# Optimization experiments

Measured on AMD Instinct MI355X. Metric: run time of the kernel, lower is better.

The kernel has to match this reference:

```python
import jax, jax.numpy as jnp
import numpy as np

B, N, M, D, H = 4, 2048, 2048, 1024, 16
HD = D // H


def setup_inputs() -> dict:
    key = jax.random.key(0)
    ks = jax.random.split(key, 16)
    s = 1.0 / np.sqrt(D)
    inp = {
        "Q": jax.random.normal(ks[0], (B, N, D), jnp.float32),
        "K": jax.random.normal(ks[1], (B, M, D), jnp.float32),
        "V": jax.random.normal(ks[2], (B, M, D), jnp.float32),
        "attn_bias": jax.random.normal(ks[3], (B, N, M), jnp.float32),
        "mask": jax.random.randint(ks[4], (B, M), 0, 2).astype(bool),
        # linear params (torch nn.Linear: y = x @ W.T + b)
        "Wq": jax.random.uniform(ks[5], (D, D), jnp.float32, -s, s),
        "bq": jax.random.uniform(ks[6], (D,), jnp.float32, -s, s),
        "Wk": jax.random.uniform(ks[7], (D, D), jnp.float32, -s, s),
        "bk": jax.random.uniform(ks[8], (D,), jnp.float32, -s, s),
        "Wv": jax.random.uniform(ks[9], (D, D), jnp.float32, -s, s),
        "bv": jax.random.uniform(ks[10], (D,), jnp.float32, -s, s),
        "Wo": jax.random.uniform(ks[11], (D, D), jnp.float32, -s, s),
        "bo": jax.random.uniform(ks[12], (D,), jnp.float32, -s, s),
    }
    return inp


def reference(Q, K, V, attn_bias, mask, Wq, bq, Wk, bk, Wv, bv, Wo, bo):
    b, n, d = Q.shape
    m = K.shape[1]
    # bias (B,N,M) -> (B,1,N,M); mask (B,M) True = masked out (-inf)
    bias = attn_bias[:, None, :, :]
    bias = jnp.where(mask[:, None, None, :], -jnp.inf, bias)
    # projections, split heads: (B, H, len, head_dim)
    q = (Q @ Wq.T + bq).reshape(b, n, H, HD).transpose(0, 2, 1, 3)
    k = (K @ Wk.T + bk).reshape(b, m, H, HD).transpose(0, 2, 1, 3)
    v = (V @ Wv.T + bv).reshape(b, m, H, HD).transpose(0, 2, 1, 3)
    scale = 1.0 / np.sqrt(HD).astype(np.float32)
    attn = jnp.einsum("bhid,bhjd->bhij", q * scale, k) + bias
    attn = jax.nn.softmax(attn, axis=-1)
    out = jnp.einsum("bhij,bhjd->bhid", attn, v)
    out = out.transpose(0, 2, 1, 3).reshape(b, n, d)
    return out @ Wo.T + bo
```

## Files before the change

kernel.cpp:

```cpp
#include <hip/hip_runtime.h>
#include <hip/hip_bf16.h>

#define Bq 4
#define Nq 2048
#define Mq 2048
#define Dq 1024
#define Hq 16

typedef __attribute__((ext_vector_type(8))) short short8;
typedef __attribute__((ext_vector_type(4))) short short4v;
typedef __attribute__((ext_vector_type(4))) float floatx4;
typedef __attribute__((ext_vector_type(16))) float floatx16;
typedef __attribute__((ext_vector_type(4))) unsigned uint4v;

static __device__ __forceinline__ short f2bf(float f) {
    __hip_bfloat16 h = __float2bfloat16(f);
    short r;
    __builtin_memcpy(&r, &h, 2);
    return r;
}
static __device__ __forceinline__ float bf2f(short s) {
    unsigned u = ((unsigned)(unsigned short)s) << 16;
    float f;
    __builtin_memcpy(&f, &u, 4);
    return f;
}
static __device__ __forceinline__ unsigned cvtpk_bf16(float lo, float hi) {
    unsigned r;
    asm("v_cvt_pk_bf16_f32 %0, %1, %2" : "=v"(r) : "v"(lo), "v"(hi));
    return r;
}
static __device__ __forceinline__ void swap32(unsigned &a, unsigned &b) {
    asm("v_permlane32_swap_b32 %0, %1" : "+v"(a), "+v"(b));
}
static __device__ __forceinline__ void gld16(const void* g, void* l) {
    __builtin_amdgcn_global_load_lds(
        (const __attribute__((address_space(1))) unsigned int*)g,
        (__attribute__((address_space(3))) unsigned int*)l, 16, 0, 0);
}

__global__ void bias_prep(const float* __restrict__ bias, const int* __restrict__ mask,
                          short* __restrict__ out)
{
    const long i = ((long)blockIdx.x * 256 + threadIdx.x) * 4;
    const int m = (int)(i & (Mq - 1));
    const int b = (int)(i >> 22);
    floatx4 v = *(const floatx4*)(bias + i);
    short4v o;
#pragma unroll
    for (int e = 0; e < 4; ++e) {
        const float t = v[e] + (mask[b * Mq + m + e] ? -1e38f : 0.0f);
        o[e] = f2bf(t);
    }
    *(short4v*)(out + i) = o;
}

template<bool A_BF16, int OMODE>
__global__ __launch_bounds__(256, 2)
void gemm_bt(const void* __restrict__ Ap, const float* __restrict__ Bp,
             const float* __restrict__ biasp, void* __restrict__ Cp, int K, float scale)
{
    __shared__ short As[128 * 32];
    __shared__ short Bs[128 * 32];
    short8* As8 = (short8*)As;
    short8* Bs8 = (short8*)Bs;

    const int tid = threadIdx.x;
    const int lane = tid & 63;
    const int wid = tid >> 6;
    const int wr = wid >> 1, wc = wid & 1;
    const int g = lane >> 4, c = lane & 15;
    const long row0 = (long)blockIdx.x * 128;
    const int col0 = blockIdx.y * 128;

    const int srow = tid >> 1;
    const int sk = (tid & 1) * 16;

    floatx4 acc[4][4];
#pragma unroll
    for (int i = 0; i < 4; ++i)
#pragma unroll
        for (int j = 0; j < 4; ++j) acc[i][j] = (floatx4)0.0f;

    for (int kt = 0; kt < K; kt += 32) {
        short8 a0, a1, b0, b1;
        if constexpr (A_BF16) {
            const short* ap = (const short*)Ap + (row0 + srow) * (long)K + kt + sk;
            a0 = *(const short8*)ap;
            a1 = *(const short8*)(ap + 8);
        } else {
            const float* ap = (const float*)Ap + (row0 + srow) * (long)K + kt + sk;
            floatx4 f0 = *(const floatx4*)ap,       f1 = *(const floatx4*)(ap + 4),
                    f2 = *(const floatx4*)(ap + 8), f3 = *(const floatx4*)(ap + 12);
#pragma unroll
            for (int e = 0; e < 4; ++e) {
                a0[e] = f2bf(f0[e]); a0[e + 4] = f2bf(f1[e]);
                a1[e] = f2bf(f2[e]); a1[e + 4] = f2bf(f3[e]);
            }
        }
        {
            const float* bp = Bp + (col0 + srow) * (long)K + kt + sk;
            floatx4 f0 = *(const floatx4*)bp,       f1 = *(const floatx4*)(bp + 4),
                    f2 = *(const floatx4*)(bp + 8), f3 = *(const floatx4*)(bp + 12);
#pragma unroll
            for (int e = 0; e < 4; ++e) {
                b0[e] = f2bf(f0[e]); b0[e + 4] = f2bf(f1[e]);
                b1[e] = f2bf(f2[e]); b1[e + 4] = f2bf(f3[e]);
            }
        }
        const int u0 = sk >> 3;
        const int sw = (srow >> 1) & 3;
        As8[srow * 4 + ((u0)     ^ sw)] = a0;
        As8[srow * 4 + ((u0 + 1) ^ sw)] = a1;
        Bs8[srow * 4 + ((u0)     ^ sw)] = b0;
        Bs8[srow * 4 + ((u0 + 1) ^ sw)] = b1;
        __syncthreads();

        short8 af[4], bfq[4];
#pragma unroll
        for (int fm = 0; fm < 4; ++fm) {
            const int r = wr * 64 + fm * 16 + c;
            af[fm] = As8[r * 4 + (g ^ ((r >> 1) & 3))];
        }
#pragma unroll
        for (int fn = 0; fn < 4; ++fn) {
            const int cc = wc * 64 + fn * 16 + c;
            bfq[fn] = Bs8[cc * 4 + (g ^ ((cc >> 1) & 3))];
        }
#pragma unroll
        for (int fm = 0; fm < 4; ++fm)
#pragma unroll
            for (int fn = 0; fn < 4; ++fn)
                acc[fm][fn] = __builtin_amdgcn_mfma_f32_16x16x32_bf16(af[fm], bfq[fn], acc[fm][fn], 0, 0, 0);
        __syncthreads();
    }

#pragma unroll
    for (int fn = 0; fn < 4; ++fn) {
        const int ccol = col0 + wc * 64 + fn * 16 + c;
        const float bv = biasp[ccol];
#pragma unroll
        for (int fm = 0; fm < 4; ++fm) {
            const long r0 = row0 + wr * 64 + fm * 16 + g * 4;
#pragma unroll
            for (int reg = 0; reg < 4; ++reg) {
                const float val = (acc[fm][fn][reg] + bv) * scale;
                const long rr = r0 + reg;
                if constexpr (OMODE == 0) {
                    ((float*)Cp)[rr * 1024 + ccol] = val;
                } else if constexpr (OMODE == 1) {
                    ((short*)Cp)[rr * 1024 + ccol] = f2bf(val);
                } else {
                    const long idx = ((long)(rr >> 11) * Dq + ccol) * (long)Mq + (rr & (Mq - 1));
                    ((short*)Cp)[idx] = f2bf(val);
                }
            }
        }
    }
}

__global__ __launch_bounds__(512, 2)
void attn_fused(const short* __restrict__ qg_, const short* __restrict__ kg_,
                const short* __restrict__ vtg, const short* __restrict__ bmg,
                short* __restrict__ outg)
{
    __shared__ __align__(16) short k_lds[64 * 64];
    __shared__ __align__(16) short v_lds[64 * 64];

    const int tid = threadIdx.x;
    const int lane = tid & 63;
    const int w = tid >> 6;
    const int hi = lane >> 5;
    const int q31 = lane & 31;

    const int blk = blockIdx.x;
    const int xcd = blk & 7, s = blk >> 3;
    const int grp = xcd * 2 + (s >> 4);
    const int b = grp >> 2, qt = grp & 3;
    const int h = s & 15;

    const long qbase = (long)b * Nq + qt * 512 + w * 64;

    short8 qf[2][4];
#pragma unroll
    for (int qg = 0; qg < 2; ++qg)
#pragma unroll
        for (int ks = 0; ks < 4; ++ks)
            qf[qg][ks] = *(const short8*)(qg_ + (qbase + qg * 32 + q31) * Dq + h * 64 + ks * 16 + hi * 8);

    floatx16 oa[2][2];
    float m_s[2], l_s[2];
#pragma unroll
    for (int qg = 0; qg < 2; ++qg) {
        m_s[qg] = -1e37f; l_s[qg] = 0.0f;
        oa[qg][0] = (floatx16)0.0f; oa[qg][1] = (floatx16)0.0f;
    }

    const int sr = tid >> 3;
    const int su = (tid & 7) ^ (sr & 7);
    const char* ksrc0 = (const char*)(kg_ + ((long)b * Mq + sr) * Dq + h * 64 + su * 8);
    const char* vsrc0 = (const char*)(vtg + ((long)b * Dq + h * 64 + sr) * Mq + su * 8);
    void* kdst = (void*)((char*)k_lds + w * 1024);
    void* vdst = (void*)((char*)v_lds + w * 1024);

    for (int kt = 0; kt < 32; ++kt) {
        const long j0 = (long)kt * 64;
        gld16(ksrc0 + j0 * (Dq * 2), kdst);
        gld16(vsrc0 + j0 * 2, vdst);
        __syncthreads();

        short8 kf[2][4];
#pragma unroll
        for (int kg = 0; kg < 2; ++kg)
#pragma unroll
            for (int ks = 0; ks < 4; ++ks) {
                const int r = kg * 32 + q31;
                const int up = (2 * ks + hi) ^ (r & 7);
                kf[kg][ks] = *(const short8*)((const char*)k_lds + r * 128 + up * 16);
            }
        floatx16 sa[2][2];
#pragma unroll
        for (int qg = 0; qg < 2; ++qg)
#pragma unroll
            for (int kg = 0; kg < 2; ++kg) {
                sa[qg][kg] = (floatx16)0.0f;
#pragma unroll
                for (int ks = 0; ks < 4; ++ks)
                    sa[qg][kg] = __builtin_amdgcn_mfma_f32_32x32x16_bf16(kf[kg][ks], qf[qg][ks], sa[qg][kg], 0, 0, 0);
            }

        short8 vf[2][4];
#pragma unroll
        for (int dg = 0; dg < 2; ++dg)
#pragma unroll
            for (int ks = 0; ks < 4; ++ks) {
                const int r = dg * 32 + q31;
                const int up = (2 * ks + hi) ^ (r & 7);
                vf[dg][ks] = *(const short8*)((const char*)v_lds + r * 128 + up * 16);
            }

#pragma unroll
        for (int qg = 0; qg < 2; ++qg) {
            const short* brow = bmg + (qbase + qg * 32 + q31) * Mq + j0;
            float p[32];
#pragma unroll
            for (int kg = 0; kg < 2; ++kg)
#pragma unroll
                for (int Qh = 0; Qh < 4; ++Qh) {
                    short4v bb = *(const short4v*)(brow + kg * 32 + Qh * 8 + hi * 4);
#pragma unroll
                    for (int e = 0; e < 4; ++e)
                        p[kg * 16 + Qh * 4 + e] = sa[qg][kg][Qh * 4 + e] + bf2f(bb[e]);
                }
            float pm = p[0];
#pragma unroll
            for (int i = 1; i < 32; ++i) pm = fmaxf(pm, p[i]);
            pm = fmaxf(pm, __shfl_xor(pm, 32));
            if (!__all(pm <= m_s[qg] + 8.0f)) {
                const float mn = fmaxf(m_s[qg], pm);
                const float al = __expf(m_s[qg] - mn);
                l_s[qg] *= al;
                oa[qg][0] *= al; oa[qg][1] *= al;
                m_s[qg] = mn;
            }
            float rs = 0.0f;
#pragma unroll
            for (int i = 0; i < 32; ++i) { p[i] = __expf(p[i] - m_s[qg]); rs += p[i]; }
            rs += __shfl_xor(rs, 32);
            l_s[qg] += rs;

            uint4v pw[4];
#pragma unroll
            for (int kg = 0; kg < 2; ++kg) {
                unsigned w0 = cvtpk_bf16(p[kg * 16 + 0], p[kg * 16 + 1]);
                unsigned w1 = cvtpk_bf16(p[kg * 16 + 2], p[kg * 16 + 3]);
                unsigned w2 = cvtpk_bf16(p[kg * 16 + 4], p[kg * 16 + 5]);
                unsigned w3 = cvtpk_bf16(p[kg * 16 + 6], p[kg * 16 + 7]);
                swap32(w0, w2); swap32(w1, w3);
                pw[kg * 2][0] = w0; pw[kg * 2][1] = w1; pw[kg * 2][2] = w2; pw[kg * 2][3] = w3;
                unsigned w4 = cvtpk_bf16(p[kg * 16 + 8],  p[kg * 16 + 9]);
                unsigned w5 = cvtpk_bf16(p[kg * 16 + 10], p[kg * 16 + 11]);
                unsigned w6 = cvtpk_bf16(p[kg * 16 + 12], p[kg * 16 + 13]);
                unsigned w7 = cvtpk_bf16(p[kg * 16 + 14], p[kg * 16 + 15]);
                swap32(w4, w6); swap32(w5, w7);
                pw[kg * 2 + 1][0] = w4; pw[kg * 2 + 1][1] = w5; pw[kg * 2 + 1][2] = w6; pw[kg * 2 + 1][3] = w7;
            }
#pragma unroll
            for (int dg = 0; dg < 2; ++dg)
#pragma unroll
                for (int ks = 0; ks < 4; ++ks)
                    oa[qg][dg] = __builtin_amdgcn_mfma_f32_32x32x16_bf16(
                        vf[dg][ks], __builtin_bit_cast(short8, pw[ks]), oa[qg][dg], 0, 0, 0);
        }
        __syncthreads();
    }

#pragma unroll
    for (int qg = 0; qg < 2; ++qg) {
        const float invl = 1.0f / l_s[qg];
        short* op = outg + (qbase + qg * 32 + q31) * Dq + h * 64;
#pragma unroll
        for (int dg = 0; dg < 2; ++dg)
#pragma unroll
            for (int Qh = 0; Qh < 4; ++Qh) {
                short4v t;
#pragma unroll
                for (int e = 0; e < 4; ++e)
                    t[e] = f2bf(oa[qg][dg][Qh * 4 + e] * invl);
                *(short4v*)(op + dg * 32 + Qh * 8 + hi * 4) = t;
            }
    }
}

extern "C" void kernel_launch(void* const* d_in, const int* in_sizes, int n_in,
                              void* d_out, int out_size, void* d_ws, size_t ws_size,
                              hipStream_t stream)
{
    const float* Q    = (const float*)d_in[0];
    const float* K    = (const float*)d_in[1];
    const float* V    = (const float*)d_in[2];
    const float* bias = (const float*)d_in[3];
    const int*   mask = (const int*)d_in[4];
    const float* Wq   = (const float*)d_in[5];
    const float* bq   = (const float*)d_in[6];
    const float* Wk   = (const float*)d_in[7];
    const float* bk   = (const float*)d_in[8];
    const float* Wv   = (const float*)d_in[9];
    const float* bv   = (const float*)d_in[10];
    const float* Wo   = (const float*)d_in[11];
    const float* bo   = (const float*)d_in[12];

    const size_t SZ = (size_t)Bq * Nq * Dq;
    short* q_ws  = (short*)d_ws;
    short* k_ws  = q_ws  + (size_t)Bq * Nq * Dq;
    short* vt_ws = k_ws  + (size_t)Bq * Mq * Dq;
    short* a_ws  = vt_ws + (size_t)Bq * Mq * Dq;
    short* bm_ws = a_ws  + (size_t)Bq * Nq * Dq;
    (void)SZ; (void)ws_size;

    bias_prep<<<dim3((Bq * Nq * Mq) / 4 / 256), dim3(256), 0, stream>>>(bias, mask, bm_ws);

    dim3 grid(64, 8);
    gemm_bt<false, 1><<<grid, 256, 0, stream>>>(Q, Wq, bq, q_ws, Dq, 0.125f);
    gemm_bt<false, 1><<<grid, 256, 0, stream>>>(K, Wk, bk, k_ws, Dq, 1.0f);
    gemm_bt<false, 2><<<grid, 256, 0, stream>>>(V, Wv, bv, vt_ws, Dq, 1.0f);
    attn_fused<<<dim3(256), dim3(512), 0, stream>>>(q_ws, k_ws, vt_ws, bm_ws, a_ws);
    gemm_bt<true, 0><<<grid, 256, 0, stream>>>(a_ws, Wo, bo, d_out, Dq, 1.0f);
}
```

Before: 359.4 us.

## Double-buffer GEMM and attention, pre-convert weights, batch QKV, use exp2 softmax

The four weight matrices are converted to bf16 once in a separate kernel, and the three QKV projections are batched into a single launch over a z grid dimension. The GEMM now double-buffers shared memory, staging weights with global-to-LDS loads so the next tile is fetched during the current MFMAs. The attention kernel is reorganised into 256-thread blocks that each process 32 queries per wave, with double-buffered K/V tiles, the bias loads hoisted ahead of the MFMAs, and tree reductions for max and sum. Softmax switches to exp2 by folding log2(e) into the Q scale and the bias, and the rescale threshold is relaxed. The trade-off is an extra conversion launch, higher LDS use, and different occupancy.

Measured after the change: 342.4 us. 1.05x faster.

```diff
diff --git a/kernel.cpp b/kernel.cpp
--- a/kernel.cpp
+++ b/kernel.cpp
@@ -33,6 +33,11 @@
 static __device__ __forceinline__ void swap32(unsigned &a, unsigned &b) {
     asm("v_permlane32_swap_b32 %0, %1" : "+v"(a), "+v"(b));
 }
+static __device__ __forceinline__ float exp2_fast(float x) {
+    float r;
+    asm("v_exp_f32 %0, %1" : "=v"(r) : "v"(x));
+    return r;
+}
 static __device__ __forceinline__ void gld16(const void* g, void* l) {
     __builtin_amdgcn_global_load_lds(
         (const __attribute__((address_space(1))) unsigned int*)g,
@@ -42,28 +47,56 @@
 __global__ void bias_prep(const float* __restrict__ bias, const int* __restrict__ mask,
                           short* __restrict__ out)
 {
-    const long i = ((long)blockIdx.x * 256 + threadIdx.x) * 4;
+    const long i = ((long)blockIdx.x * 256 + threadIdx.x) * 8;
     const int m = (int)(i & (Mq - 1));
     const int b = (int)(i >> 22);
-    floatx4 v = *(const floatx4*)(bias + i);
-    short4v o;
+    floatx4 f0 = *(const floatx4*)(bias + i);
+    floatx4 f1 = *(const floatx4*)(bias + i + 4);
+    const int* mp = mask + b * Mq + m;
+    short8 o;
 #pragma unroll
     for (int e = 0; e < 4; ++e) {
-        const float t = v[e] + (mask[b * Mq + m + e] ? -1e38f : 0.0f);
-        o[e] = f2bf(t);
-    }
-    *(short4v*)(out + i) = o;
-}
-
-template<bool A_BF16, int OMODE>
-__global__ __launch_bounds__(256, 2)
-void gemm_bt(const void* __restrict__ Ap, const float* __restrict__ Bp,
-             const float* __restrict__ biasp, void* __restrict__ Cp, int K, float scale)
+        o[e]     = mp[e]     ? f2bf(-1e38f) : f2bf(f0[e] * 1.44269504f);
+        o[e + 4] = mp[e + 4] ? f2bf(-1e38f) : f2bf(f1[e] * 1.44269504f);
+    }
+    *(short8*)(out + i) = o;
+}
+
+__global__ void cvt_w(const float* __restrict__ w0, const float* __restrict__ w1,
+                      const float* __restrict__ w2, const float* __restrict__ w3,
+                      short* __restrict__ out)
 {
-    __shared__ short As[128 * 32];
-    __shared__ short Bs[128 * 32];
-    short8* As8 = (short8*)As;
-    short8* Bs8 = (short8*)Bs;
+    const int z = blockIdx.y;
+    const float* s = (z == 0) ? w0 : (z == 1) ? w1 : (z == 2) ? w2 : w3;
+    short* d = out + (size_t)z * (Dq * Dq);
+    const int i = (blockIdx.x * 256 + threadIdx.x) * 8;
+    floatx4 f0 = *(const floatx4*)(s + i);
+    floatx4 f1 = *(const floatx4*)(s + i + 4);
+    short8 o;
+#pragma unroll
+    for (int e = 0; e < 4; ++e) { o[e] = f2bf(f0[e]); o[e + 4] = f2bf(f1[e]); }
+    *(short8*)(d + i) = o;
+}
+
+struct GB {
+    const void* A[3];
+    const short* W[3];
+    const float* bias[3];
+    void* C[3];
+    float scale[3];
+    int omode[3];
+};
+
+template<bool ABF>
+__global__ __launch_bounds__(256, 3)
+void gemm_bt(GB gb, int K)
+{
+    __shared__ __align__(16) short As[2][128 * 32];
+    __shared__ __align__(16) short Bs[2][128 * 32];
+
+    const int z = blockIdx.z;
+    const char* Ap = (const char*)gb.A[z];
+    const short* Wp = gb.W[z];
 
     const int tid = threadIdx.x;
     const int lane = tid & 63;
@@ -75,6 +108,9 @@
 
     const int srow = tid >> 1;
     const int sk = (tid & 1) * 16;
+    const int R0 = tid >> 2;
+    const int ub = (tid & 3) ^ ((R0 >> 1) & 3);
+    const short* bsrc = Wp + ((long)col0 + R0) * K + ub * 8;
 
     floatx4 acc[4][4];
 #pragma unroll
@@ -82,14 +118,18 @@
 #pragma unroll
         for (int j = 0; j < 4; ++j) acc[i][j] = (floatx4)0.0f;
 
-    for (int kt = 0; kt < K; kt += 32) {
-        short8 a0, a1, b0, b1;
-        if constexpr (A_BF16) {
-            const short* ap = (const short*)Ap + (row0 + srow) * (long)K + kt + sk;
-            a0 = *(const short8*)ap;
-            a1 = *(const short8*)(ap + 8);
+    {
+        char* d0 = (char*)Bs + wid * 1024;
+        gld16(bsrc, d0);
+        gld16(bsrc + 64L * K, d0 + 4096);
+    }
+    {
+        short8 a0, a1;
+        if constexpr (ABF) {
+            const short* ap = (const short*)Ap + (row0 + srow) * (long)K + sk;
+            a0 = *(const short8*)ap; a1 = *(const short8*)(ap + 8);
         } else {
-            const float* ap = (const float*)Ap + (row0 + srow) * (long)K + kt + sk;
+            const float* ap = (const float*)Ap + (row0 + srow) * (long)K + sk;
             floatx4 f0 = *(const floatx4*)ap,       f1 = *(const floatx4*)(ap + 4),
                     f2 = *(const floatx4*)(ap + 8), f3 = *(const floatx4*)(ap + 12);
 #pragma unroll
@@ -98,24 +138,33 @@
                 a1[e] = f2bf(f2[e]); a1[e + 4] = f2bf(f3[e]);
             }
         }
-        {
-            const float* bp = Bp + (col0 + srow) * (long)K + kt + sk;
-            floatx4 f0 = *(const floatx4*)bp,       f1 = *(const floatx4*)(bp + 4),
-                    f2 = *(const floatx4*)(bp + 8), f3 = *(const floatx4*)(bp + 12);
-#pragma unroll
-            for (int e = 0; e < 4; ++e) {
-                b0[e] = f2bf(f0[e]); b0[e + 4] = f2bf(f1[e]);
-                b1[e] = f2bf(f2[e]); b1[e + 4] = f2bf(f3[e]);
-            }
-        }
-        const int u0 = sk >> 3;
-        const int sw = (srow >> 1) & 3;
+        short8* As8 = (short8*)As;
+        const int u0 = sk >> 3, sw = (srow >> 1) & 3;
         As8[srow * 4 + ((u0)     ^ sw)] = a0;
         As8[srow * 4 + ((u0 + 1) ^ sw)] = a1;
-        Bs8[srow * 4 + ((u0)     ^ sw)] = b0;
-        Bs8[srow * 4 + ((u0 + 1) ^ sw)] = b1;
-        __syncthreads();
-
+    }
+    __syncthreads();
+
+    int buf = 0;
+    for (int kt = 0; kt < K; kt += 32) {
+        const bool nlast = (kt + 32 < K);
+        floatx4 f0, f1, f2, f3;
+        short8 s0, s1;
+        if (nlast) {
+            char* d0 = (char*)Bs + (buf ^ 1) * 8192 + wid * 1024;
+            gld16(bsrc + kt + 32, d0);
+            gld16(bsrc + 64L * K + kt + 32, d0 + 4096);
+            if constexpr (ABF) {
+                const short* ap = (const short*)Ap + (row0 + srow) * (long)K + kt + 32 + sk;
+                s0 = *(const short8*)ap; s1 = *(const short8*)(ap + 8);
+            } else {
+                const float* ap = (const float*)Ap + (row0 + srow) * (long)K + kt + 32 + sk;
+                f0 = *(const floatx4*)ap;       f1 = *(const floatx4*)(ap + 4);
+                f2 = *(const floatx4*)(ap + 8); f3 = *(const floatx4*)(ap + 12);
+            }
+        }
+        short8* As8 = (short8*)((char*)As + buf * 8192);
+        short8* Bs8 = (short8*)((char*)Bs + buf * 8192);
         short8 af[4], bfq[4];
 #pragma unroll
         for (int fm = 0; fm < 4; ++fm) {
@@ -132,40 +181,60 @@
 #pragma unroll
             for (int fn = 0; fn < 4; ++fn)
                 acc[fm][fn] = __builtin_amdgcn_mfma_f32_16x16x32_bf16(af[fm], bfq[fn], acc[fm][fn], 0, 0, 0);
+        if (nlast) {
+            short8 a0, a1;
+            if constexpr (ABF) { a0 = s0; a1 = s1; }
+            else {
+#pragma unroll
+                for (int e = 0; e < 4; ++e) {
+                    a0[e] = f2bf(f0[e]); a0[e + 4] = f2bf(f1[e]);
+                    a1[e] = f2bf(f2[e]); a1[e + 4] = f2bf(f3[e]);
+                }
+            }
+            short8* An8 = (short8*)((char*)As + (buf ^ 1) * 8192);
+            const int u0 = sk >> 3, sw = (srow >> 1) & 3;
+            An8[srow * 4 + ((u0)     ^ sw)] = a0;
+            An8[srow * 4 + ((u0 + 1) ^ sw)] = a1;
+        }
         __syncthreads();
-    }
-
+        buf ^= 1;
+    }
+
+    const float sc = gb.scale[z];
+    const float* bp = gb.bias[z];
+    const int om = gb.omode[z];
+    void* Cp = gb.C[z];
 #pragma unroll
     for (int fn = 0; fn < 4; ++fn) {
         const int ccol = col0 + wc * 64 + fn * 16 + c;
-        const float bv = biasp[ccol];
+        const float bv = bp[ccol];
 #pragma unroll
         for (int fm = 0; fm < 4; ++fm) {
             const long r0 = row0 + wr * 64 + fm * 16 + g * 4;
 #pragma unroll
             for (int reg = 0; reg < 4; ++reg) {
-                const float val = (acc[fm][fn][reg] + bv) * scale;
+                const float val = (acc[fm][fn][reg] + bv) * sc;
                 const long rr = r0 + reg;
-                if constexpr (OMODE == 0) {
-                    ((float*)Cp)[rr * 1024 + ccol] = val;
-                } else if constexpr (OMODE == 1) {
-                    ((short*)Cp)[rr * 1024 + ccol] = f2bf(val);
-                } else {
+                if (om == 0) {
+                    ((short*)Cp)[rr * Dq + ccol] = f2bf(val);
+                } else if (om == 1) {
                     const long idx = ((long)(rr >> 11) * Dq + ccol) * (long)Mq + (rr & (Mq - 1));
                     ((short*)Cp)[idx] = f2bf(val);
+                } else {
+                    ((float*)Cp)[rr * Dq + ccol] = val;
                 }
             }
         }
     }
 }
 
-__global__ __launch_bounds__(512, 2)
+__global__ __launch_bounds__(256, 4)
 void attn_fused(const short* __restrict__ qg_, const short* __restrict__ kg_,
                 const short* __restrict__ vtg, const short* __restrict__ bmg,
                 short* __restrict__ outg)
 {
-    __shared__ __align__(16) short k_lds[64 * 64];
-    __shared__ __align__(16) short v_lds[64 * 64];
+    __shared__ __align__(16) short k_lds[2][64 * 64];
+    __shared__ __align__(16) short v_lds[2][64 * 64];
 
     const int tid = threadIdx.x;
     const int lane = tid & 63;
@@ -174,142 +243,154 @@
     const int q31 = lane & 31;
 
     const int blk = blockIdx.x;
-    const int xcd = blk & 7, s = blk >> 3;
-    const int grp = xcd * 2 + (s >> 4);
-    const int b = grp >> 2, qt = grp & 3;
-    const int h = s & 15;
-
-    const long qbase = (long)b * Nq + qt * 512 + w * 64;
-
-    short8 qf[2][4];
-#pragma unroll
-    for (int qg = 0; qg < 2; ++qg)
-#pragma unroll
-        for (int ks = 0; ks < 4; ++ks)
-            qf[qg][ks] = *(const short8*)(qg_ + (qbase + qg * 32 + q31) * Dq + h * 64 + ks * 16 + hi * 8);
-
-    floatx16 oa[2][2];
-    float m_s[2], l_s[2];
-#pragma unroll
-    for (int qg = 0; qg < 2; ++qg) {
-        m_s[qg] = -1e37f; l_s[qg] = 0.0f;
-        oa[qg][0] = (floatx16)0.0f; oa[qg][1] = (floatx16)0.0f;
-    }
+    const int bh = blk & 63;
+    const int qt = blk >> 6;
+    const int b = bh >> 4, h = bh & 15;
+
+    const long qbase = (long)b * Nq + qt * 128 + w * 32;
+
+    short8 qf[4];
+#pragma unroll
+    for (int ks = 0; ks < 4; ++ks)
+        qf[ks] = *(const short8*)(qg_ + (qbase + q31) * Dq + h * 64 + ks * 16 + hi * 8);
+
+    floatx16 oa[2];
+    oa[0] = (floatx16)0.0f; oa[1] = (floatx16)0.0f;
+    float m_s = -1e37f, l_s = 0.0f;
 
     const int sr = tid >> 3;
     const int su = (tid & 7) ^ (sr & 7);
-    const char* ksrc0 = (const char*)(kg_ + ((long)b * Mq + sr) * Dq + h * 64 + su * 8);
-    const char* vsrc0 = (const char*)(vtg + ((long)b * Dq + h * 64 + sr) * Mq + su * 8);
-    void* kdst = (void*)((char*)k_lds + w * 1024);
-    void* vdst = (void*)((char*)v_lds + w * 1024);
-
+    const char* ksrc = (const char*)(kg_ + ((long)b * Mq + sr) * Dq + h * 64 + su * 8);
+    const char* vsrc = (const char*)(vtg + ((long)b * Dq + h * 64 + sr) * Mq + su * 8);
+
+#define STAGE(bf, kt2) do {                                                   \
+        const long j0b = (long)(kt2) * 64;                                    \
+        char* kd = (char*)k_lds + (bf) * 8192 + w * 1024;                     \
+        char* vd = (char*)v_lds + (bf) * 8192 + w * 1024;                     \
+        gld16(ksrc + j0b * (Dq * 2), kd);                                     \
+        gld16(ksrc + (j0b + 32) * (Dq * 2), kd + 4096);                       \
+        gld16(vsrc + j0b * 2, vd);                                            \
+        gld16(vsrc + 32L * Mq * 2 + j0b * 2, vd + 4096);                      \
+    } while (0)
+
+    STAGE(0, 0);
+    __syncthreads();
+
+    int buf = 0;
     for (int kt = 0; kt < 32; ++kt) {
-        const long j0 = (long)kt * 64;
-        gld16(ksrc0 + j0 * (Dq * 2), kdst);
-        gld16(vsrc0 + j0 * 2, vdst);
-        __syncthreads();
-
-        short8 kf[2][4];
+        if (kt < 31) STAGE(buf ^ 1, kt + 1);
+        const short* brow = bmg + (qbase + q31) * Mq + (long)kt * 64;
+        short4v bb[8];
 #pragma unroll
         for (int kg = 0; kg < 2; ++kg)
+#pragma unroll
+            for (int Qh = 0; Qh < 4; ++Qh)
+                bb[kg * 4 + Qh] = *(const short4v*)(brow + kg * 32 + Qh * 8 + hi * 4);
+
+        const char* kb = (const char*)k_lds + buf * 8192;
+        const char* vb = (const char*)v_lds + buf * 8192;
+
+        floatx16 sa[2];
+#pragma unroll
+        for (int kg = 0; kg < 2; ++kg) {
+            short8 kf[4];
 #pragma unroll
             for (int ks = 0; ks < 4; ++ks) {
                 const int r = kg * 32 + q31;
                 const int up = (2 * ks + hi) ^ (r & 7);
-                kf[kg][ks] = *(const short8*)((const char*)k_lds + r * 128 + up * 16);
-            }
-        floatx16 sa[2][2];
-#pragma unroll
-        for (int qg = 0; qg < 2; ++qg)
-#pragma unroll
-            for (int kg = 0; kg < 2; ++kg) {
-                sa[qg][kg] = (floatx16)0.0f;
-#pragma unroll
-                for (int ks = 0; ks < 4; ++ks)
-                    sa[qg][kg] = __builtin_amdgcn_mfma_f32_32x32x16_bf16(kf[kg][ks], qf[qg][ks], sa[qg][kg], 0, 0, 0);
-            }
-
-        short8 vf[2][4];
-#pragma unroll
-        for (int dg = 0; dg < 2; ++dg)
+                kf[ks] = *(const short8*)(kb + r * 128 + up * 16);
+            }
+            sa[kg] = (floatx16)0.0f;
+#pragma unroll
+            for (int ks = 0; ks < 4; ++ks)
+                sa[kg] = __builtin_amdgcn_mfma_f32_32x32x16_bf16(kf[ks], qf[ks], sa[kg], 0, 0, 0);
+        }
+
+        float p[32];
+#pragma unroll
+        for (int kg = 0; kg < 2; ++kg)
+#pragma unroll
+            for (int Qh = 0; Qh < 4; ++Qh) {
+                const short4v bv4 = bb[kg * 4 + Qh];
+#pragma unroll
+                for (int e = 0; e < 4; ++e)
+                    p[kg * 16 + Qh * 4 + e] = sa[kg][Qh * 4 + e] + bf2f(bv4[e]);
+            }
+        float t16[16];
+#pragma unroll
+        for (int i = 0; i < 16; ++i) t16[i] = fmaxf(p[2 * i], p[2 * i + 1]);
+#pragma unroll
+        for (int i = 0; i < 8; ++i) t16[i] = fmaxf(t16[2 * i], t16[2 * i + 1]);
+        t16[0] = fmaxf(fmaxf(fmaxf(t16[0], t16[1]), fmaxf(t16[2], t16[3])),
+                       fmaxf(fmaxf(t16[4], t16[5]), fmaxf(t16[6], t16[7])));
+        const float pm = fmaxf(t16[0], __shfl_xor(t16[0], 32));
+        if (!__all(pm <= m_s + 11.5f)) {
+            const float mn = fmaxf(m_s, pm);
+            const float al = exp2_fast(m_s - mn);
+            l_s *= al;
+            oa[0] *= al; oa[1] *= al;
+            m_s = mn;
+        }
+#pragma unroll
+        for (int i = 0; i < 32; ++i) p[i] = exp2_fast(p[i] - m_s);
+        float s16[16];
+#pragma unroll
+        for (int i = 0; i < 16; ++i) s16[i] = p[2 * i] + p[2 * i + 1];
+#pragma unroll
+        for (int i = 0; i < 8; ++i) s16[i] = s16[2 * i] + s16[2 * i + 1];
+        float rs = ((s16[0] + s16[1]) + (s16[2] + s16[3])) +
+                   ((s16[4] + s16[5]) + (s16[6] + s16[7]));
+        rs += __shfl_xor(rs, 32);
+        l_s += rs;
+
+        uint4v pw[4];
+#pragma unroll
+        for (int kg = 0; kg < 2; ++kg) {
+            unsigned w0 = cvtpk_bf16(p[kg * 16 + 0], p[kg * 16 + 1]);
+            unsigned w1 = cvtpk_bf16(p[kg * 16 + 2], p[kg * 16 + 3]);
+            unsigned w2 = cvtpk_bf16(p[kg * 16 + 4], p[kg * 16 + 5]);
+            unsigned w3 = cvtpk_bf16(p[kg * 16 + 6], p[kg * 16 + 7]);
+            swap32(w0, w2); swap32(w1, w3);
+            pw[kg * 2][0] = w0; pw[kg * 2][1] = w1; pw[kg * 2][2] = w2; pw[kg * 2][3] = w3;
+            unsigned w4 = cvtpk_bf16(p[kg * 16 + 8],  p[kg * 16 + 9]);
+            unsigned w5 = cvtpk_bf16(p[kg * 16 + 10], p[kg * 16 + 11]);
+            unsigned w6 = cvtpk_bf16(p[kg * 16 + 12], p[kg * 16 + 13]);
+            unsigned w7 = cvtpk_bf16(p[kg * 16 + 14], p[kg * 16 + 15]);
+            swap32(w4, w6); swap32(w5, w7);
+            pw[kg * 2 + 1][0] = w4; pw[kg * 2 + 1][1] = w5; pw[kg * 2 + 1][2] = w6; pw[kg * 2 + 1][3] = w7;
+        }
+
+#pragma unroll
+        for (int dg = 0; dg < 2; ++dg) {
+            short8 vf[4];
 #pragma unroll
             for (int ks = 0; ks < 4; ++ks) {
                 const int r = dg * 32 + q31;
                 const int up = (2 * ks + hi) ^ (r & 7);
-                vf[dg][ks] = *(const short8*)((const char*)v_lds + r * 128 + up * 16);
-            }
-
-#pragma unroll
-        for (int qg = 0; qg < 2; ++qg) {
-            const short* brow = bmg + (qbase + qg * 32 + q31) * Mq + j0;
-            float p[32];
-#pragma unroll
-            for (int kg = 0; kg < 2; ++kg)
-#pragma unroll
-                for (int Qh = 0; Qh < 4; ++Qh) {
-                    short4v bb = *(const short4v*)(brow + kg * 32 + Qh * 8 + hi * 4);
-#pragma unroll
-                    for (int e = 0; e < 4; ++e)
-                        p[kg * 16 + Qh * 4 + e] = sa[qg][kg][Qh * 4 + e] + bf2f(bb[e]);
-                }
-            float pm = p[0];
-#pragma unroll
-            for (int i = 1; i < 32; ++i) pm = fmaxf(pm, p[i]);
-            pm = fmaxf(pm, __shfl_xor(pm, 32));
-            if (!__all(pm <= m_s[qg] + 8.0f)) {
-                const float mn = fmaxf(m_s[qg], pm);
-                const float al = __expf(m_s[qg] - mn);
-                l_s[qg] *= al;
-                oa[qg][0] *= al; oa[qg][1] *= al;
-                m_s[qg] = mn;
-            }
-            float rs = 0.0f;
-#pragma unroll
-            for (int i = 0; i < 32; ++i) { p[i] = __expf(p[i] - m_s[qg]); rs += p[i]; }
-            rs += __shfl_xor(rs, 32);
-            l_s[qg] += rs;
-
-            uint4v pw[4];
-#pragma unroll
-            for (int kg = 0; kg < 2; ++kg) {
-                unsigned w0 = cvtpk_bf16(p[kg * 16 + 0], p[kg * 16 + 1]);
-                unsigned w1 = cvtpk_bf16(p[kg * 16 + 2], p[kg * 16 + 3]);
-                unsigned w2 = cvtpk_bf16(p[kg * 16 + 4], p[kg * 16 + 5]);
-                unsigned w3 = cvtpk_bf16(p[kg * 16 + 6], p[kg * 16 + 7]);
-                swap32(w0, w2); swap32(w1, w3);
-                pw[kg * 2][0] = w0; pw[kg * 2][1] = w1; pw[kg * 2][2] = w2; pw[kg * 2][3] = w3;
-                unsigned w4 = cvtpk_bf16(p[kg * 16 + 8],  p[kg * 16 + 9]);
-                unsigned w5 = cvtpk_bf16(p[kg * 16 + 10], p[kg * 16 + 11]);
-                unsigned w6 = cvtpk_bf16(p[kg * 16 + 12], p[kg * 16 + 13]);
-                unsigned w7 = cvtpk_bf16(p[kg * 16 + 14], p[kg * 16 + 15]);
-                swap32(w4, w6); swap32(w5, w7);
-                pw[kg * 2 + 1][0] = w4; pw[kg * 2 + 1][1] = w5; pw[kg * 2 + 1][2] = w6; pw[kg * 2 + 1][3] = w7;
-            }
-#pragma unroll
-            for (int dg = 0; dg < 2; ++dg)
-#pragma unroll
-                for (int ks = 0; ks < 4; ++ks)
-                    oa[qg][dg] = __builtin_amdgcn_mfma_f32_32x32x16_bf16(
-                        vf[dg][ks], __builtin_bit_cast(short8, pw[ks]), oa[qg][dg], 0, 0, 0);
+                vf[ks] = *(const short8*)(vb + r * 128 + up * 16);
+            }
+#pragma unroll
+            for (int ks = 0; ks < 4; ++ks)
+                oa[dg] = __builtin_amdgcn_mfma_f32_32x32x16_bf16(
+                    vf[ks], __builtin_bit_cast(short8, pw[ks]), oa[dg], 0, 0, 0);
         }
         __syncthreads();
-    }
-
-#pragma unroll
-    for (int qg = 0; qg < 2; ++qg) {
-        const float invl = 1.0f / l_s[qg];
-        short* op = outg + (qbase + qg * 32 + q31) * Dq + h * 64;
-#pragma unroll
-        for (int dg = 0; dg < 2; ++dg)
-#pragma unroll
-            for (int Qh = 0; Qh < 4; ++Qh) {
-                short4v t;
-#pragma unroll
-                for (int e = 0; e < 4; ++e)
-                    t[e] = f2bf(oa[qg][dg][Qh * 4 + e] * invl);
-                *(short4v*)(op + dg * 32 + Qh * 8 + hi * 4) = t;
-            }
-    }
+        buf ^= 1;
+    }
+#undef STAGE
+
+    const float invl = 1.0f / l_s;
+    short* op = outg + (qbase + q31) * Dq + h * 64;
+#pragma unroll
+    for (int dg = 0; dg < 2; ++dg)
+#pragma unroll
+        for (int Qh = 0; Qh < 4; ++Qh) {
+            short4v t;
+#pragma unroll
+            for (int e = 0; e < 4; ++e)
+                t[e] = f2bf(oa[dg][Qh * 4 + e] * invl);
+            *(short4v*)(op + dg * 32 + Qh * 8 + hi * 4) = t;
+        }
 }
 
 extern "C" void kernel_launch(void* const* d_in, const int* in_sizes, int n_in,
@@ -330,20 +411,35 @@
     const float* Wo   = (const float*)d_in[11];
     const float* bo   = (const float*)d_in[12];
 
-    const size_t SZ = (size_t)Bq * Nq * Dq;
+    const size_t TSZ = (size_t)Bq * Nq * Dq;
     short* q_ws  = (short*)d_ws;
-    short* k_ws  = q_ws  + (size_t)Bq * Nq * Dq;
-    short* vt_ws = k_ws  + (size_t)Bq * Mq * Dq;
-    short* a_ws  = vt_ws + (size_t)Bq * Mq * Dq;
-    short* bm_ws = a_ws  + (size_t)Bq * Nq * Dq;
-    (void)SZ; (void)ws_size;
-
-    bias_prep<<<dim3((Bq * Nq * Mq) / 4 / 256), dim3(256), 0, stream>>>(bias, mask, bm_ws);
-
-    dim3 grid(64, 8);
-    gemm_bt<false, 1><<<grid, 256, 0, stream>>>(Q, Wq, bq, q_ws, Dq, 0.125f);
-    gemm_bt<false, 1><<<grid, 256, 0, stream>>>(K, Wk, bk, k_ws, Dq, 1.0f);
-    gemm_bt<false, 2><<<grid, 256, 0, stream>>>(V, Wv, bv, vt_ws, Dq, 1.0f);
-    attn_fused<<<dim3(256), dim3(512), 0, stream>>>(q_ws, k_ws, vt_ws, bm_ws, a_ws);
-    gemm_bt<true, 0><<<grid, 256, 0, stream>>>(a_ws, Wo, bo, d_out, Dq, 1.0f);
-}
+    short* k_ws  = q_ws  + TSZ;
+    short* vt_ws = k_ws  + TSZ;
+    short* a_ws  = vt_ws + TSZ;
+    short* bm_ws = a_ws  + TSZ;
+    short* w_ws  = bm_ws + (size_t)Bq * Nq * Mq;
+    (void)ws_size;
+
+    bias_prep<<<dim3(8192), dim3(256), 0, stream>>>(bias, mask, bm_ws);
+    cvt_w<<<dim3(512, 4), dim3(256), 0, stream>>>(Wq, Wk, Wv, Wo, w_ws);
+
+    GB g1{};
+    g1.A[0] = Q;  g1.A[1] = K;  g1.A[2] = V;
+    g1.W[0] = w_ws; g1.W[1] = w_ws + Dq * Dq; g1.W[2] = w_ws + 2 * Dq * Dq;
+    g1.bias[0] = bq; g1.bias[1] = bk; g1.bias[2] = bv;
+    g1.C[0] = q_ws; g1.C[1] = k_ws; g1.C[2] = vt_ws;
+    g1.scale[0] = 0.125f * 1.44269504f; g1.scale[1] = 1.0f; g1.scale[2] = 1.0f;
+    g1.omode[0] = 0; g1.omode[1] = 0; g1.omode[2] = 1;
+    gemm_bt<false><<<dim3(64, 8, 3), dim3(256), 0, stream>>>(g1, Dq);
+
+    attn_fused<<<dim3(1024), dim3(256), 0, stream>>>(q_ws, k_ws, vt_ws, bm_ws, a_ws);
+
+    GB g2{};
+    g2.A[0] = a_ws;
+    g2.W[0] = w_ws + 3 * Dq * Dq;
+    g2.bias[0] = bo;
+    g2.C[0] = d_out;
+    g2.scale[0] = 1.0f;
+    g2.omode[0] = 2;
+    gemm_bt<true><<<dim3(64, 8, 1), dim3(256), 0, stream>>>(g2, Dq);
+}
```
